# Kernel tuning notes

Measured on AMD Instinct MI355X. Metric: run time of the kernel, lower is better.

## Reference

```python
import jax, jax.numpy as jnp
import numpy as np

EMB = 1024
HID = 4096
B = 2
T = 4096
NUM_BLOCK = 24
EPS = 1e-6


def rmsnorm(x):
    # unparameterized RMS normalization over last dim
    return x * jax.lax.rsqrt(jnp.mean(jnp.square(x), axis=-1, keepdims=True) + EPS)


def setup_inputs() -> dict:
    key = jax.random.key(0)
    k1, k2, k3, k4 = jax.random.split(key, 4)
    x = jax.random.normal(k1, (B, T, EMB), dtype=jnp.float32)
    W1 = 0.02 * jax.random.normal(k2, (HID, EMB), dtype=jnp.float32)
    W2 = 0.02 * jax.random.normal(k3, (HID, EMB), dtype=jnp.float32)
    W3 = (0.02 / np.sqrt(NUM_BLOCK)) * jax.random.normal(k4, (EMB, HID), dtype=jnp.float32)
    return {"x": x, "W1": W1, "W2": W2, "W3": W3}


def bar_quadratic_causal_preact_stable(a, b):
    # y_t = (1/t^2) * sum_{i<=t} sum_{j<=t} exp(a_i + b_j), per feature channel.
    # exp factorizes, so compute stably via log-cumsum-exp along the seq axis.
    seq = a.shape[1]
    log_t = jnp.log(jnp.arange(1, seq + 1, dtype=a.dtype))  # [T]
    la = jax.lax.cumlogsumexp(a, axis=1)  # [B,T,H]
    lb = jax.lax.cumlogsumexp(b, axis=1)  # [B,T,H]
    return jnp.exp(la + lb - 2.0 * log_t[None, :, None])


def reference(x, W1, W2, W3):
    r = rmsnorm(x)
    a = jnp.einsum('bte,he->bth', r, W1)  # fc_1, no bias
    b = jnp.einsum('bte,he->bth', r, W2)  # fc_2, no bias
    r = bar_quadratic_causal_preact_stable(a, b)
    r = rmsnorm(r)
    r = jnp.einsum('bth,eh->bte', r, W3)  # fc_3, no bias
    return x + r
```

## Files before the change

kernel.cpp:

```cpp
#include <hip/hip_runtime.h>
#include <hip/hip_fp8.h>

#define EMB 1024
#define HID 4096
#define NB 2
#define TT 4096
#define MROWS (NB*TT)
#define N1 (2*HID)
#define CHUNK 128
#define NCH 32

typedef short short8 __attribute__((ext_vector_type(8)));
typedef float v4f   __attribute__((ext_vector_type(4)));

__device__ __forceinline__ unsigned short f2bf(float f) {
  unsigned int u = __float_as_uint(f);
  u += 0x7FFFu + ((u >> 16) & 1u);
  return (unsigned short)(u >> 16);
}
__device__ __forceinline__ float bf2f(unsigned short s) {
  return __uint_as_float(((unsigned int)s) << 16);
}
__device__ __forceinline__ float h2f(unsigned short u) {
  return (float)(*(const _Float16*)&u);
}
__device__ __forceinline__ unsigned char f2e4m3(float f) {
  __hip_fp8_e4m3 q(f);
  return *(unsigned char*)&q;
}
__device__ __forceinline__ float e4m32f(unsigned char c) {
  __hip_fp8_e4m3 q = *(__hip_fp8_e4m3*)&c;
  return (float)q;
}
__device__ __forceinline__ void g2l16(const void* g, void* l) {
  __builtin_amdgcn_global_load_lds(
      (const __attribute__((address_space(1))) void*)g,
      (__attribute__((address_space(3))) void*)l, 16, 0, 0);
}

__device__ __forceinline__ float block_reduce_sum(float v, float* sbuf) {
  #pragma unroll
  for (int off = 32; off; off >>= 1) v += __shfl_down(v, off, 64);
  int lane = threadIdx.x & 63, w = threadIdx.x >> 6;
  if (lane == 0) sbuf[w] = v;
  __syncthreads();
  return sbuf[0] + sbuf[1] + sbuf[2] + sbuf[3];
}

__global__ __launch_bounds__(256) void conv_all(const float* __restrict__ W1,
                                                const float* __restrict__ W2,
                                                const float* __restrict__ W3,
                                                unsigned short* __restrict__ o12,
                                                unsigned char* __restrict__ o3) {
  size_t i = ((size_t)blockIdx.x*256 + threadIdx.x)*4;
  if (i < 2ull*HID*EMB) {
    const float* s = (i < (size_t)HID*EMB) ? (W1 + i) : (W2 + (i - (size_t)HID*EMB));
    float4 v = *(const float4*)s;
    ushort4 u; u.x=f2bf(v.x); u.y=f2bf(v.y); u.z=f2bf(v.z); u.w=f2bf(v.w);
    *(ushort4*)(o12 + i) = u;
  } else {
    size_t off = i - 2ull*HID*EMB;
    float4 v = *(const float4*)(W3 + off);
    uchar4 u; u.x=f2e4m3(v.x*64.f); u.y=f2e4m3(v.y*64.f);
             u.z=f2e4m3(v.z*64.f); u.w=f2e4m3(v.w*64.f);
    *(uchar4*)(o3 + off) = u;
  }
}

__global__ __launch_bounds__(256) void rmsnorm_x(const float* __restrict__ x,
                                                 unsigned short* __restrict__ r) {
  __shared__ float sbuf[4];
  int row = blockIdx.x;
  float4 v = *(const float4*)(x + (size_t)row*EMB + threadIdx.x*4);
  float ss = v.x*v.x + v.y*v.y + v.z*v.z + v.w*v.w;
  float tot = block_reduce_sum(ss, sbuf);
  float sc = rsqrtf(tot * (1.0f/EMB) + 1e-6f);
  ushort4 o; o.x=f2bf(v.x*sc); o.y=f2bf(v.y*sc); o.z=f2bf(v.z*sc); o.w=f2bf(v.w*sc);
  *(ushort4*)(r + (size_t)row*EMB + threadIdx.x*4) = o;
}

__global__ __launch_bounds__(256) void normq(const unsigned short* __restrict__ y,
                                             unsigned char* __restrict__ y8) {
  __shared__ float sbuf[4];
  int row = blockIdx.x;
  const unsigned short* p = y + (size_t)row*HID + threadIdx.x*16;
  short8 v0 = *(const short8*)p;
  short8 v1 = *(const short8*)(p+8);
  float f[16]; float ss = 0.f;
  #pragma unroll
  for (int j=0;j<8;++j){ f[j]=bf2f((unsigned short)v0[j]); f[j+8]=bf2f((unsigned short)v1[j]); }
  #pragma unroll
  for (int j=0;j<16;++j) ss += f[j]*f[j];
  float tot = block_reduce_sum(ss, sbuf);
  float sc = rsqrtf(tot*(1.0f/HID) + 1e-6f);
  unsigned int w[4];
  #pragma unroll
  for (int g=0; g<4; ++g) {
    unsigned int a0 = f2e4m3(f[g*4+0]*sc);
    unsigned int a1 = f2e4m3(f[g*4+1]*sc);
    unsigned int a2 = f2e4m3(f[g*4+2]*sc);
    unsigned int a3 = f2e4m3(f[g*4+3]*sc);
    w[g] = a0 | (a1<<8) | (a2<<16) | (a3<<24);
  }
  uint4 o; o.x=w[0]; o.y=w[1]; o.z=w[2]; o.w=w[3];
  *(uint4*)(y8 + (size_t)row*HID + threadIdx.x*16) = o;
}

__global__ __launch_bounds__(256, 2)
void gemm_exp(const unsigned short* __restrict__ A,
              const unsigned short* __restrict__ Bt,
              unsigned char* __restrict__ C8,
              float* __restrict__ part,
              int K, int N) {
  __shared__ short lA[128*64];
  __shared__ short lB[128*64];
  const int tid  = threadIdx.x;
  const int lane = tid & 63;
  const int wm   = (tid >> 6) >> 1, wn = (tid >> 6) & 1;
  const int bid  = blockIdx.x;
  const int s0i  = bid >> 3;
  const int rowTile = s0i >> 3;
  const int colTile = ((bid & 7) << 3) | (s0i & 7);
  const int rowBase = rowTile * 128;
  const int colBase = colTile * 128;

  v4f acc[4][4];
  #pragma unroll
  for (int i=0;i<4;++i)
    #pragma unroll
    for (int j=0;j<4;++j) acc[i][j] = (v4f){0.f,0.f,0.f,0.f};

  for (int k0 = 0; k0 < K; k0 += 64) {
    #pragma unroll
    for (int j = 0; j < 4; ++j) {
      int s = j*256 + tid;
      int m = s >> 3;
      int c = (s & 7) ^ (m & 7);
      g2l16(A + (size_t)(rowBase + m)*K + k0 + c*8, &lA[s*8]);
    }
    #pragma unroll
    for (int j = 0; j < 4; ++j) {
      int s = j*256 + tid;
      int m = s >> 3;
      int c = (s & 7) ^ (m & 7);
      g2l16(Bt + (size_t)(colBase + m)*K + k0 + c*8, &lB[s*8]);
    }
    __syncthreads();
    #pragma unroll
    for (int s2 = 0; s2 < 2; ++s2) {
      const int quad = lane >> 4;
      const int cc = s2*4 + quad;
      short8 aF[4], bF[4];
      #pragma unroll
      for (int mt = 0; mt < 4; ++mt) {
        int ml = wm*64 + mt*16 + (lane & 15);
        aF[mt] = *(const short8*)&lA[(ml*8 + (cc ^ (ml & 7)))*8];
      }
      #pragma unroll
      for (int nt = 0; nt < 4; ++nt) {
        int nl = wn*64 + nt*16 + (lane & 15);
        bF[nt] = *(const short8*)&lB[(nl*8 + (cc ^ (nl & 7)))*8];
      }
      #pragma unroll
      for (int mt = 0; mt < 4; ++mt)
        #pragma unroll
        for (int nt = 0; nt < 4; ++nt)
          acc[mt][nt] = __builtin_amdgcn_mfma_f32_16x16x32_bf16(aF[mt], bF[nt], acc[mt][nt], 0, 0, 0);
    }
    __syncthreads();
  }

  const int quad = lane >> 4, c15 = lane & 15;
  float csum[4] = {0.f, 0.f, 0.f, 0.f};
  #pragma unroll
  for (int mt = 0; mt < 4; ++mt) {
    #pragma unroll
    for (int nt = 0; nt < 4; ++nt) {
      int col = colBase + wn*64 + nt*16 + c15;
      #pragma unroll
      for (int r = 0; r < 4; ++r) {
        int row = rowBase + wm*64 + mt*16 + quad*4 + r;
        size_t idx = (size_t)row*N + col;
        float e = __expf(acc[mt][nt][r]);
        C8[idx] = f2e4m3(e);
        csum[nt] += e;
      }
    }
  }
  float* cs = (float*)lA;
  #pragma unroll
  for (int nt = 0; nt < 4; ++nt) {
    float s = csum[nt];
    s += __shfl_xor(s, 16, 64);
    s += __shfl_xor(s, 32, 64);
    if (lane < 16) cs[wm*128 + wn*64 + nt*16 + lane] = s;
  }
  __syncthreads();
  if (tid < 128)
    part[(size_t)(colBase + tid)*64 + rowTile] = cs[tid] + cs[128 + tid];
}

__global__ __launch_bounds__(256, 2)
void gemm_out(const unsigned char* __restrict__ A8,
              const unsigned char* __restrict__ B8,
              unsigned short* __restrict__ Ph,
              int K, int KCH, int N) {
  __shared__ unsigned char lA8[128*128];
  __shared__ unsigned char lB8[128*128];
  const int tid  = threadIdx.x;
  const int lane = tid & 63;
  const int wm   = (tid >> 6) >> 1, wn = (tid >> 6) & 1;
  const int rowBase = blockIdx.x * 128;
  const int colBase = blockIdx.y * 128;
  const int kStart  = blockIdx.z * KCH;

  v4f acc[4][4];
  #pragma unroll
  for (int i=0;i<4;++i)
    #pragma unroll
    for (int j=0;j<4;++j) acc[i][j] = (v4f){0.f,0.f,0.f,0.f};

  for (int k0 = kStart; k0 < kStart + KCH; k0 += 128) {
    #pragma unroll
    for (int j = 0; j < 4; ++j) {
      int s = j*256 + tid;
      int m = s >> 3;
      int c = (s & 7) ^ (m & 7);
      g2l16(A8 + (size_t)(rowBase + m)*K + k0 + c*16, &lA8[s*16]);
    }
    #pragma unroll
    for (int j = 0; j < 4; ++j) {
      int s = j*256 + tid;
      int m = s >> 3;
      int c = (s & 7) ^ (m & 7);
      g2l16(B8 + (size_t)(colBase + m)*K + k0 + c*16, &lB8[s*16]);
    }
    __syncthreads();
    #pragma unroll
    for (int s2 = 0; s2 < 4; ++s2) {
      const int quad = lane >> 4;
      const int cc = s2*2 + (quad >> 1);
      const int hh = quad & 1;
      long aF[4], bF[4];
      #pragma unroll
      for (int mt = 0; mt < 4; ++mt) {
        int ml = wm*64 + mt*16 + (lane & 15);
        aF[mt] = *(const long*)&lA8[ml*128 + ((cc ^ (ml & 7))<<4) + (hh<<3)];
      }
      #pragma unroll
      for (int nt = 0; nt < 4; ++nt) {
        int nl = wn*64 + nt*16 + (lane & 15);
        bF[nt] = *(const long*)&lB8[nl*128 + ((cc ^ (nl & 7))<<4) + (hh<<3)];
      }
      #pragma unroll
      for (int mt = 0; mt < 4; ++mt)
        #pragma unroll
        for (int nt = 0; nt < 4; ++nt)
          acc[mt][nt] = __builtin_amdgcn_mfma_f32_16x16x32_fp8_fp8(aF[mt], bF[nt], acc[mt][nt], 0, 0, 0);
    }
    __syncthreads();
  }

  const int quad = lane >> 4, c15 = lane & 15;
  #pragma unroll
  for (int mt = 0; mt < 4; ++mt) {
    #pragma unroll
    for (int nt = 0; nt < 4; ++nt) {
      int col = colBase + wn*64 + nt*16 + c15;
      #pragma unroll
      for (int r = 0; r < 4; ++r) {
        int row = rowBase + wm*64 + mt*16 + quad*4 + r;
        size_t idx = ((size_t)blockIdx.z*MROWS + row)*N + col;
        _Float16 h = (_Float16)acc[mt][nt][r];
        Ph[idx] = *(unsigned short*)&h;
      }
    }
  }
}

__global__ __launch_bounds__(256) void scan_prefix(float* __restrict__ part) {
  int idx = blockIdx.x*256 + threadIdx.x;
  int col = idx >> 1, bb = idx & 1;
  float* p = part + (size_t)col*64 + bb*NCH;
  float run = 0.f;
  #pragma unroll
  for (int c = 0; c < NCH; ++c) { float v = p[c]; p[c] = run; run += v; }
}

__global__ __launch_bounds__(256) void scan_emit(const unsigned char* __restrict__ ab,
                                                 const float* __restrict__ part,
                                                 unsigned short* __restrict__ y) {
  int h = blockIdx.x*256 + threadIdx.x;
  int cy = blockIdx.y, bb = blockIdx.z;
  float sa = part[(size_t)h*64 + bb*NCH + cy];
  float sb = part[(size_t)(HID + h)*64 + bb*NCH + cy];
  const unsigned char* pa = ab + ((size_t)(bb*TT + cy*CHUNK))*N1 + h;
  const unsigned char* pb = pa + HID;
  unsigned short* py = y + ((size_t)(bb*TT + cy*CHUNK))*HID + h;
  int t0 = cy*CHUNK;
  #pragma unroll 4
  for (int i = 0; i < CHUNK; ++i) {
    sa += e4m32f(pa[(size_t)i*N1]);
    sb += e4m32f(pb[(size_t)i*N1]);
    float inv = 1.0f / (float)(t0 + i + 1);
    py[(size_t)i*HID] = f2bf(sa*sb*inv*inv);
  }
}

__global__ __launch_bounds__(256) void reduce_out(const unsigned short* __restrict__ p,
                                                  const float* __restrict__ x,
                                                  float* __restrict__ o) {
  size_t i = ((size_t)blockIdx.x*256 + threadIdx.x)*4;
  float4 xv = *(const float4*)(x + i);
  float s0 = 0.f, s1 = 0.f, s2 = 0.f, s3 = 0.f;
  #pragma unroll
  for (int z = 0; z < 4; ++z) {
    ushort4 u = *(const ushort4*)(p + (size_t)z*MROWS*EMB + i);
    s0 += h2f(u.x); s1 += h2f(u.y); s2 += h2f(u.z); s3 += h2f(u.w);
  }
  const float inv64 = 1.0f/64.0f;
  float4 ov; ov.x = xv.x + inv64*s0; ov.y = xv.y + inv64*s1;
             ov.z = xv.z + inv64*s2; ov.w = xv.w + inv64*s3;
  *(float4*)(o + i) = ov;
}

extern "C" void kernel_launch(void* const* d_in, const int* in_sizes, int n_in,
                              void* d_out, int out_size, void* d_ws, size_t ws_size,
                              hipStream_t stream) {
  const float* x  = (const float*)d_in[0];
  const float* W1 = (const float*)d_in[1];
  const float* W2 = (const float*)d_in[2];
  const float* W3 = (const float*)d_in[3];
  float* out = (float*)d_out;
  char* ws = (char*)d_ws;

  unsigned short* r_bf   = (unsigned short*)(ws);
  unsigned short* w12_bf = (unsigned short*)(ws + 16777216ull);
  unsigned char*  w3_8   = (unsigned char*) (ws + 33554432ull);
  unsigned char*  ab8    = (unsigned char*) (ws + 37748736ull);
  unsigned short* y_bf   = (unsigned short*)(ws + 104857600ull);
  unsigned char*  y8     = (unsigned char*) (ws + 171966464ull);
  unsigned short* psum   = (unsigned short*)ab8;
  float*          part   = (float*)d_out;

  conv_all<<<12288, 256, 0, stream>>>(W1, W2, W3, w12_bf, w3_8);
  rmsnorm_x<<<MROWS, 256, 0, stream>>>(x, r_bf);
  gemm_exp<<<4096, 256, 0, stream>>>(r_bf, w12_bf, ab8, part, EMB, N1);
  scan_prefix<<<64, 256, 0, stream>>>(part);
  scan_emit<<<dim3(16,NCH,2), 256, 0, stream>>>(ab8, part, y_bf);
  normq<<<MROWS, 256, 0, stream>>>(y_bf, y8);
  gemm_out<<<dim3(64,8,4), 256, 0, stream>>>(y8, w3_8, psum, HID, 1024, EMB);
  reduce_out<<<8192, 256, 0, stream>>>(psum, x, out);
}
```

Measured before the change: 381.0 us.

## Restructure fc1/fc2 GEMM into 256x256 tiles with 4-stage async LDS pipeline

The fused exp GEMM now uses 512-thread blocks computing 256x256 output tiles instead of 128x128. Global-to-LDS loads run through a 4-buffer ring with two stages of lookahead, gated by explicit vmcnt waits and a single barrier per K step, and setprio is raised around the MFMA burst. This aims to hide load latency and raise MFMA utilization through larger tiles and more data reuse. The column partial sums are written per 128-row chunk directly, so the LDS reduction is dropped. The cost is higher register pressure (8x4 accumulators) and 128KB of LDS per block, which may limit occupancy.

```diff
diff --git a/kernel.cpp b/kernel.cpp
--- a/kernel.cpp
+++ b/kernel.cpp
@@ -106,98 +106,126 @@
   *(uint4*)(y8 + (size_t)row*HID + threadIdx.x*16) = o;
 }
 
-__global__ __launch_bounds__(256, 2)
+__global__ __launch_bounds__(512, 2)
 void gemm_exp(const unsigned short* __restrict__ A,
               const unsigned short* __restrict__ Bt,
               unsigned char* __restrict__ C8,
               float* __restrict__ part,
               int K, int N) {
-  __shared__ short lA[128*64];
-  __shared__ short lB[128*64];
+  __shared__ short lds[4][2][256*32];
   const int tid  = threadIdx.x;
   const int lane = tid & 63;
-  const int wm   = (tid >> 6) >> 1, wn = (tid >> 6) & 1;
+  const int wid  = tid >> 6;
+  const int wr   = wid >> 2;
+  const int wc   = wid & 3;
   const int bid  = blockIdx.x;
-  const int s0i  = bid >> 3;
-  const int rowTile = s0i >> 3;
-  const int colTile = ((bid & 7) << 3) | (s0i & 7);
-  const int rowBase = rowTile * 128;
-  const int colBase = colTile * 128;
-
-  v4f acc[4][4];
-  #pragma unroll
-  for (int i=0;i<4;++i)
+  const int s0   = bid >> 3;
+  const int colTile = ((bid & 7) << 2) | (s0 & 3);
+  const int rowTile = s0 >> 2;
+  const int rowBase = rowTile << 8;
+  const int colBase = colTile << 8;
+  const int NT = K >> 5;
+
+  v4f acc[8][4];
+  #pragma unroll
+  for (int i=0;i<8;++i)
     #pragma unroll
     for (int j=0;j<4;++j) acc[i][j] = (v4f){0.f,0.f,0.f,0.f};
 
-  for (int k0 = 0; k0 < K; k0 += 64) {
-    #pragma unroll
-    for (int j = 0; j < 4; ++j) {
-      int s = j*256 + tid;
-      int m = s >> 3;
-      int c = (s & 7) ^ (m & 7);
-      g2l16(A + (size_t)(rowBase + m)*K + k0 + c*8, &lA[s*8]);
-    }
-    #pragma unroll
-    for (int j = 0; j < 4; ++j) {
-      int s = j*256 + tid;
-      int m = s >> 3;
-      int c = (s & 7) ^ (m & 7);
-      g2l16(Bt + (size_t)(colBase + m)*K + k0 + c*8, &lB[s*8]);
-    }
-    __syncthreads();
-    #pragma unroll
-    for (int s2 = 0; s2 < 2; ++s2) {
-      const int quad = lane >> 4;
-      const int cc = s2*4 + quad;
-      short8 aF[4], bF[4];
-      #pragma unroll
-      for (int mt = 0; mt < 4; ++mt) {
-        int ml = wm*64 + mt*16 + (lane & 15);
-        aF[mt] = *(const short8*)&lA[(ml*8 + (cc ^ (ml & 7)))*8];
-      }
-      #pragma unroll
-      for (int nt = 0; nt < 4; ++nt) {
-        int nl = wn*64 + nt*16 + (lane & 15);
-        bF[nt] = *(const short8*)&lB[(nl*8 + (cc ^ (nl & 7)))*8];
-      }
-      #pragma unroll
-      for (int mt = 0; mt < 4; ++mt)
-        #pragma unroll
-        for (int nt = 0; nt < 4; ++nt)
-          acc[mt][nt] = __builtin_amdgcn_mfma_f32_16x16x32_bf16(aF[mt], bF[nt], acc[mt][nt], 0, 0, 0);
-    }
-    __syncthreads();
-  }
-
-  const int quad = lane >> 4, c15 = lane & 15;
+  auto stage = [&](int t) {
+    const int buf = t & 3;
+    const int k0  = t << 5;
+    #pragma unroll
+    for (int j = 0; j < 2; ++j) {
+      int slot = j*512 + tid;
+      int msw  = slot >> 2;
+      int m    = msw ^ ((msw >> 2) & 1);
+      int c    = (slot & 3) ^ (m & 3);
+      g2l16(A + (size_t)(rowBase + m)*K + k0 + c*8, &lds[buf][0][slot*8]);
+    }
+    #pragma unroll
+    for (int j = 0; j < 2; ++j) {
+      int slot = j*512 + tid;
+      int msw  = slot >> 2;
+      int m    = msw ^ ((msw >> 2) & 1);
+      int c    = (slot & 3) ^ (m & 3);
+      g2l16(Bt + (size_t)(colBase + m)*K + k0 + c*8, &lds[buf][1][slot*8]);
+    }
+  };
+
+  stage(0);
+  if (NT > 1) stage(1);
+
+  const int q   = lane >> 4;
+  const int r15 = lane & 15;
+
+  for (int t = 0; t < NT; ++t) {
+    if (t + 2 < NT) stage(t + 2);
+    if (t + 2 < NT)      asm volatile("s_waitcnt vmcnt(8)" ::: "memory");
+    else if (t + 1 < NT) asm volatile("s_waitcnt vmcnt(4)" ::: "memory");
+    else                 asm volatile("s_waitcnt vmcnt(0)" ::: "memory");
+    __builtin_amdgcn_s_barrier();
+    __builtin_amdgcn_sched_barrier(0);
+
+    const short* lA = &lds[t & 3][0][0];
+    const short* lB = &lds[t & 3][1][0];
+    short8 aF[4], bF[4], aG[4];
+    #pragma unroll
+    for (int mt = 0; mt < 4; ++mt) {
+      int m = wr*128 + mt*16 + r15;
+      int slot = ((m ^ ((m >> 2) & 1)) << 2) | (q ^ (m & 3));
+      aF[mt] = *(const short8*)&lA[slot*8];
+    }
+    #pragma unroll
+    for (int nt = 0; nt < 4; ++nt) {
+      int n = wc*64 + nt*16 + r15;
+      int slot = ((n ^ ((n >> 2) & 1)) << 2) | (q ^ (n & 3));
+      bF[nt] = *(const short8*)&lB[slot*8];
+    }
+    #pragma unroll
+    for (int mt = 0; mt < 4; ++mt) {
+      int m = wr*128 + (mt+4)*16 + r15;
+      int slot = ((m ^ ((m >> 2) & 1)) << 2) | (q ^ (m & 3));
+      aG[mt] = *(const short8*)&lA[slot*8];
+    }
+    __builtin_amdgcn_s_setprio(1);
+    #pragma unroll
+    for (int mt = 0; mt < 4; ++mt)
+      #pragma unroll
+      for (int nt = 0; nt < 4; ++nt)
+        acc[mt][nt] = __builtin_amdgcn_mfma_f32_16x16x32_bf16(aF[mt], bF[nt], acc[mt][nt], 0, 0, 0);
+    #pragma unroll
+    for (int mt = 0; mt < 4; ++mt)
+      #pragma unroll
+      for (int nt = 0; nt < 4; ++nt)
+        acc[mt+4][nt] = __builtin_amdgcn_mfma_f32_16x16x32_bf16(aG[mt], bF[nt], acc[mt+4][nt], 0, 0, 0);
+    __builtin_amdgcn_s_setprio(0);
+  }
+
   float csum[4] = {0.f, 0.f, 0.f, 0.f};
   #pragma unroll
-  for (int mt = 0; mt < 4; ++mt) {
+  for (int mt = 0; mt < 8; ++mt) {
     #pragma unroll
     for (int nt = 0; nt < 4; ++nt) {
-      int col = colBase + wn*64 + nt*16 + c15;
-      #pragma unroll
-      for (int r = 0; r < 4; ++r) {
-        int row = rowBase + wm*64 + mt*16 + quad*4 + r;
-        size_t idx = (size_t)row*N + col;
-        float e = __expf(acc[mt][nt][r]);
-        C8[idx] = f2e4m3(e);
+      int col = colBase + wc*64 + nt*16 + r15;
+      #pragma unroll
+      for (int rr = 0; rr < 4; ++rr) {
+        int row = rowBase + wr*128 + mt*16 + q*4 + rr;
+        float e = __expf(acc[mt][nt][rr]);
+        C8[(size_t)row*N + col] = f2e4m3(e);
         csum[nt] += e;
       }
     }
   }
-  float* cs = (float*)lA;
+  const int chunk = rowTile*2 + wr;
   #pragma unroll
   for (int nt = 0; nt < 4; ++nt) {
-    float s = csum[nt];
-    s += __shfl_xor(s, 16, 64);
-    s += __shfl_xor(s, 32, 64);
-    if (lane < 16) cs[wm*128 + wn*64 + nt*16 + lane] = s;
-  }
-  __syncthreads();
-  if (tid < 128)
-    part[(size_t)(colBase + tid)*64 + rowTile] = cs[tid] + cs[128 + tid];
+    float v = csum[nt];
+    v += __shfl_xor(v, 16, 64);
+    v += __shfl_xor(v, 32, 64);
+    if (lane < 16)
+      part[(size_t)(colBase + wc*64 + nt*16 + lane)*64 + chunk] = v;
+  }
 }
 
 __global__ __launch_bounds__(256, 2)
@@ -345,7 +373,7 @@
 
   conv_all<<<12288, 256, 0, stream>>>(W1, W2, W3, w12_bf, w3_8);
   rmsnorm_x<<<MROWS, 256, 0, stream>>>(x, r_bf);
-  gemm_exp<<<4096, 256, 0, stream>>>(r_bf, w12_bf, ab8, part, EMB, N1);
+  gemm_exp<<<1024, 512, 0, stream>>>(r_bf, w12_bf, ab8, part, EMB, N1);
   scan_prefix<<<64, 256, 0, stream>>>(part);
   scan_emit<<<dim3(16,NCH,2), 256, 0, stream>>>(ab8, part, y_bf);
   normq<<<MROWS, 256, 0, stream>>>(y_bf, y8);
```

New measurement: 384.4 us. About the same (+0.9%).

## Drop split-K in output GEMM and fuse residual add into its epilogue

Applied to the files above, without the earlier changes.

The output GEMM no longer splits K four ways into fp16 partial buffers that a separate reduce kernel sums. Each block now runs the full K loop and writes x plus the scaled accumulator straight to the output. This removes the partial-sum write/read traffic and one kernel launch. The cost is a grid of 512 blocks instead of 2048, which lowers parallelism and can leave CUs underused.

```diff
diff --git a/kernel.cpp b/kernel.cpp
--- a/kernel.cpp
+++ b/kernel.cpp
@@ -20,9 +20,6 @@
 }
 __device__ __forceinline__ float bf2f(unsigned short s) {
   return __uint_as_float(((unsigned int)s) << 16);
-}
-__device__ __forceinline__ float h2f(unsigned short u) {
-  return (float)(*(const _Float16*)&u);
 }
 __device__ __forceinline__ unsigned char f2e4m3(float f) {
   __hip_fp8_e4m3 q(f);
@@ -203,8 +200,9 @@
 __global__ __launch_bounds__(256, 2)
 void gemm_out(const unsigned char* __restrict__ A8,
               const unsigned char* __restrict__ B8,
-              unsigned short* __restrict__ Ph,
-              int K, int KCH, int N) {
+              const float* __restrict__ x,
+              float* __restrict__ out,
+              int K, int N) {
   __shared__ unsigned char lA8[128*128];
   __shared__ unsigned char lB8[128*128];
   const int tid  = threadIdx.x;
@@ -212,7 +210,6 @@
   const int wm   = (tid >> 6) >> 1, wn = (tid >> 6) & 1;
   const int rowBase = blockIdx.x * 128;
   const int colBase = blockIdx.y * 128;
-  const int kStart  = blockIdx.z * KCH;
 
   v4f acc[4][4];
   #pragma unroll
@@ -220,7 +217,7 @@
     #pragma unroll
     for (int j=0;j<4;++j) acc[i][j] = (v4f){0.f,0.f,0.f,0.f};
 
-  for (int k0 = kStart; k0 < kStart + KCH; k0 += 128) {
+  for (int k0 = 0; k0 < K; k0 += 128) {
     #pragma unroll
     for (int j = 0; j < 4; ++j) {
       int s = j*256 + tid;
@@ -262,6 +259,7 @@
   }
 
   const int quad = lane >> 4, c15 = lane & 15;
+  const float inv64 = 1.0f/64.0f;
   #pragma unroll
   for (int mt = 0; mt < 4; ++mt) {
     #pragma unroll
@@ -270,9 +268,8 @@
       #pragma unroll
       for (int r = 0; r < 4; ++r) {
         int row = rowBase + wm*64 + mt*16 + quad*4 + r;
-        size_t idx = ((size_t)blockIdx.z*MROWS + row)*N + col;
-        _Float16 h = (_Float16)acc[mt][nt][r];
-        Ph[idx] = *(unsigned short*)&h;
+        size_t idx = (size_t)row*N + col;
+        out[idx] = x[idx] + inv64*acc[mt][nt][r];
       }
     }
   }
@@ -307,23 +304,6 @@
   }
 }
 
-__global__ __launch_bounds__(256) void reduce_out(const unsigned short* __restrict__ p,
-                                                  const float* __restrict__ x,
-                                                  float* __restrict__ o) {
-  size_t i = ((size_t)blockIdx.x*256 + threadIdx.x)*4;
-  float4 xv = *(const float4*)(x + i);
-  float s0 = 0.f, s1 = 0.f, s2 = 0.f, s3 = 0.f;
-  #pragma unroll
-  for (int z = 0; z < 4; ++z) {
-    ushort4 u = *(const ushort4*)(p + (size_t)z*MROWS*EMB + i);
-    s0 += h2f(u.x); s1 += h2f(u.y); s2 += h2f(u.z); s3 += h2f(u.w);
-  }
-  const float inv64 = 1.0f/64.0f;
-  float4 ov; ov.x = xv.x + inv64*s0; ov.y = xv.y + inv64*s1;
-             ov.z = xv.z + inv64*s2; ov.w = xv.w + inv64*s3;
-  *(float4*)(o + i) = ov;
-}
-
 extern "C" void kernel_launch(void* const* d_in, const int* in_sizes, int n_in,
                               void* d_out, int out_size, void* d_ws, size_t ws_size,
                               hipStream_t stream) {
@@ -340,7 +320,6 @@
   unsigned char*  ab8    = (unsigned char*) (ws + 37748736ull);
   unsigned short* y_bf   = (unsigned short*)(ws + 104857600ull);
   unsigned char*  y8     = (unsigned char*) (ws + 171966464ull);
-  unsigned short* psum   = (unsigned short*)ab8;
   float*          part   = (float*)d_out;
 
   conv_all<<<12288, 256, 0, stream>>>(W1, W2, W3, w12_bf, w3_8);
@@ -349,6 +328,5 @@
   scan_prefix<<<64, 256, 0, stream>>>(part);
   scan_emit<<<dim3(16,NCH,2), 256, 0, stream>>>(ab8, part, y_bf);
   normq<<<MROWS, 256, 0, stream>>>(y_bf, y8);
-  gemm_out<<<dim3(64,8,4), 256, 0, stream>>>(y8, w3_8, psum, HID, 1024, EMB);
-  reduce_out<<<8192, 256, 0, stream>>>(psum, x, out);
-}
+  gemm_out<<<dim3(64,8), 256, 0, stream>>>(y8, w3_8, x, out, HID, EMB);
+}
```

Result: no change. 373.9 us (-1.9%).
